# Performance work log

Hardware: AMD Instinct MI355X
Metric: run time of the kernel (lower is better)

The kernel has to match this reference:

```python
import jax, jax.numpy as jnp
import numpy as np

B, H = 8192, 768


def _mk_linear(key, fan_in, fan_out):
    k1, k2 = jax.random.split(key)
    lim = 1.0 / np.sqrt(fan_in)
    W = jax.random.uniform(k1, (fan_out, fan_in), jnp.float32, -lim, lim)
    b = jax.random.uniform(k2, (fan_out,), jnp.float32, -lim, lim)
    return W, b


def setup_inputs() -> dict:
    key = jax.random.key(0)
    ks = jax.random.split(key, 6)
    modal_a = jax.random.normal(ks[0], (B, H), jnp.float32)
    modal_b = jax.random.normal(ks[1], (B, H), jnp.float32)
    W1m, b1m = _mk_linear(ks[2], H, H)
    W2m, b2m = _mk_linear(ks[3], H, H)
    W1v, b1v = _mk_linear(ks[4], H, H)
    W2v, b2v = _mk_linear(ks[5], H, H)
    return {"modal_a": modal_a, "modal_b": modal_b,
            "W1m": W1m, "b1m": b1m, "W2m": W2m, "b2m": b2m,
            "W1v": W1v, "b1v": b1v, "W2v": W2v, "b2v": b2v}


def reference(modal_a, modal_b, W1m, b1m, W2m, b2m, W1v, b1v, W2v, b2v):
    # mlp_mu: Linear -> Tanh -> Linear
    mu = jnp.tanh(modal_a @ W1m.T + b1m) @ W2m.T + b2m              # [B,H]
    # mlp_logvar: Linear -> Tanh -> Linear -> Tanh
    logvar = jnp.tanh(jnp.tanh(modal_a @ W1v.T + b1v) @ W2v.T + b2v)  # [B,H]
    inv_var = jnp.exp(-logvar)

    positive = -(mu - modal_b) ** 2 * 0.5 * inv_var                  # [B,H]

    # mean_j (mu[j] - mu[i])^2 = E[mu^2] - 2*mu[i]*E[mu] + mu[i]^2  (per feature dim)
    # Algebraic reduction of the O(B^2*H) tile in the original code.
    mu_mean = jnp.mean(mu, axis=0)                                   # [H]
    mu_sq_mean = jnp.mean(mu * mu, axis=0)                           # [H]
    pair_sq = mu_sq_mean - 2.0 * mu * mu_mean + mu * mu              # [B,H]
    negative = -pair_sq * 0.5 * inv_var                              # [B,H]

    pos_sum = jnp.sum(positive, axis=-1)                             # [B]
    neg_sum = jnp.sum(negative, axis=-1)                             # [B]
    lld = jnp.mean(pos_sum)
    bound = jnp.mean(pos_sum - neg_sum)
    return (lld, bound)
```

## Files before the change

kernel.cpp:

```cpp
#include <hip/hip_runtime.h>
#include <hip/hip_fp8.h>
#include <math.h>

typedef float v4f __attribute__((ext_vector_type(4)));

static constexpr int Bn = 8192;
static constexpr int Hn = 768;
static constexpr float invB = 1.0f / 8192.0f;

__device__ __forceinline__ unsigned char cvt_e4m3(float x) {
    __hip_fp8_e4m3 t(x);
    return t.__x;
}

__device__ __forceinline__ unsigned pack4_e4m3(float4 f) {
    return (unsigned)cvt_e4m3(f.x)
         | ((unsigned)cvt_e4m3(f.y) << 8)
         | ((unsigned)cvt_e4m3(f.z) << 16)
         | ((unsigned)cvt_e4m3(f.w) << 24);
}

__device__ __forceinline__ float fast_tanh(float x) {
    float xc = fminf(fmaxf(x, -15.0f), 15.0f);
    float e = __expf(2.0f * xc);
    float r = __builtin_amdgcn_rcpf(e + 1.0f);
    return 1.0f - 2.0f * r;
}

__global__ void prep_w(const float* __restrict__ W1m, const float* __restrict__ W2m,
                       const float* __restrict__ W1v, const float* __restrict__ W2v,
                       unsigned char* __restrict__ W1m_f8, unsigned char* __restrict__ W2m_f8,
                       unsigned char* __restrict__ W1v_f8, unsigned char* __restrict__ W2v_f8,
                       float* __restrict__ zbuf, int nzero) {
    const int tid = blockIdx.x * blockDim.x + threadIdx.x;
    if (tid < nzero) zbuf[tid] = 0.0f;
    constexpr int W4 = Hn * Hn / 4;
    const int total = 4 * W4;
    const int stride = gridDim.x * blockDim.x;
    for (int i = tid; i < total; i += stride) {
        int w = i / W4, j = i - w * W4;
        const float* s = (w == 0) ? W1m : (w == 1) ? W2m : (w == 2) ? W1v : W2v;
        unsigned char* d = (w == 0) ? W1m_f8 : (w == 1) ? W2m_f8 : (w == 2) ? W1v_f8 : W2v_f8;
        float4 v = ((const float4*)s)[j];
        ((unsigned*)d)[j] = pack4_e4m3(v);
    }
}

__launch_bounds__(512, 2)
__global__ void club_fused(const float* __restrict__ A_g,
                           const unsigned char* __restrict__ W1m, const unsigned char* __restrict__ W1v,
                           const unsigned char* __restrict__ W2m, const unsigned char* __restrict__ W2v,
                           const float* __restrict__ b1m, const float* __restrict__ b1v,
                           const float* __restrict__ b2m, const float* __restrict__ b2v,
                           const float* __restrict__ mb,
                           float* __restrict__ cs, float* __restrict__ cs2,
                           float* __restrict__ siv, float* __restrict__ sivmu,
                           float* __restrict__ accum, float* __restrict__ outp) {
    __shared__ __align__(16) unsigned char Hm[32 * 768];
    __shared__ __align__(16) unsigned char Xs[32 * 768];
    const int t = threadIdx.x;
    const int strip0 = blockIdx.x * 32;

    {
        const int row = t >> 4, seg = t & 15;
        const float* src = A_g + (size_t)(strip0 + row) * Hn;
#pragma unroll
        for (int j = 0; j < 3; ++j) {
            const int c = seg + 16 * j;
            float4 f0 = *(const float4*)(src + c * 16 + 0);
            float4 f1 = *(const float4*)(src + c * 16 + 4);
            float4 f2 = *(const float4*)(src + c * 16 + 8);
            float4 f3 = *(const float4*)(src + c * 16 + 12);
            uint4 p;
            p.x = pack4_e4m3(f0); p.y = pack4_e4m3(f1);
            p.z = pack4_e4m3(f2); p.w = pack4_e4m3(f3);
            *(uint4*)&Xs[row * 768 + ((c ^ (row & 15)) << 4)] = p;
        }
    }
    __syncthreads();

    const int w = t >> 6, lane = t & 63;
    const int lr = lane & 15, quad = lane >> 4;
    const int wc0 = w * 96;

    v4f am[6][2] = {}, av[6][2] = {};
    {
        ulonglong2 Wm1[2][6], Wv1[2][6];
        const unsigned char* __restrict__ pWm = W1m + (size_t)(wc0 + lr) * Hn + quad * 16;
        const unsigned char* __restrict__ pWv = W1v + (size_t)(wc0 + lr) * Hn + quad * 16;

#define LDW1(s_, ms_) do {                                                                  \
    _Pragma("unroll")                                                                       \
    for (int ct = 0; ct < 6; ++ct) {                                                        \
        Wm1[s_][ct] = *(const ulonglong2*)(pWm + ct * (16 * Hn) + (ms_) * 64);              \
        Wv1[s_][ct] = *(const ulonglong2*)(pWv + ct * (16 * Hn) + (ms_) * 64);              \
    } } while (0)

#define FM1(s_, ms_) do {                                                                   \
    ulonglong2 Af[2];                                                                       \
    _Pragma("unroll")                                                                       \
    for (int rt = 0; rt < 2; ++rt) {                                                        \
        const int row_ = rt * 16 + lr;                                                      \
        const int k_ = (ms_) * 4 + quad;                                                    \
        Af[rt] = *(const ulonglong2*)&Xs[row_ * 768 + ((k_ ^ (row_ & 15)) << 4)];           \
    }                                                                                       \
    _Pragma("unroll")                                                                       \
    for (int ct = 0; ct < 6; ++ct)                                                          \
    _Pragma("unroll")                                                                       \
    for (int rt = 0; rt < 2; ++rt) {                                                        \
        am[ct][rt] = __builtin_amdgcn_mfma_f32_16x16x32_fp8_fp8((long)Wm1[s_][ct].x, (long)Af[rt].x, am[ct][rt], 0, 0, 0); \
        am[ct][rt] = __builtin_amdgcn_mfma_f32_16x16x32_fp8_fp8((long)Wm1[s_][ct].y, (long)Af[rt].y, am[ct][rt], 0, 0, 0); \
        av[ct][rt] = __builtin_amdgcn_mfma_f32_16x16x32_fp8_fp8((long)Wv1[s_][ct].x, (long)Af[rt].x, av[ct][rt], 0, 0, 0); \
        av[ct][rt] = __builtin_amdgcn_mfma_f32_16x16x32_fp8_fp8((long)Wv1[s_][ct].y, (long)Af[rt].y, av[ct][rt], 0, 0, 0); \
    } } while (0)

        LDW1(0, 0);
#pragma unroll
        for (int ms = 0; ms < 11; ++ms) {
            if ((ms & 1) == 0) { LDW1(1, ms + 1); FM1(0, ms); }
            else               { LDW1(0, ms + 1); FM1(1, ms); }
        }
        FM1(1, 11);
#undef LDW1
#undef FM1
    }

    __syncthreads();

#pragma unroll
    for (int ct = 0; ct < 6; ++ct) {
        const float4 bbm = *(const float4*)&b1m[wc0 + ct * 16 + quad * 4];
        const float4 bbv = *(const float4*)&b1v[wc0 + ct * 16 + quad * 4];
        const int cc = w * 6 + ct;
#pragma unroll
        for (int rt = 0; rt < 2; ++rt) {
            const int row = rt * 16 + lr;
            v4f a = am[ct][rt];
            unsigned pm = (unsigned)cvt_e4m3(fast_tanh(a[0] + bbm.x))
                        | ((unsigned)cvt_e4m3(fast_tanh(a[1] + bbm.y)) << 8)
                        | ((unsigned)cvt_e4m3(fast_tanh(a[2] + bbm.z)) << 16)
                        | ((unsigned)cvt_e4m3(fast_tanh(a[3] + bbm.w)) << 24);
            v4f b = av[ct][rt];
            unsigned pv = (unsigned)cvt_e4m3(fast_tanh(b[0] + bbv.x))
                        | ((unsigned)cvt_e4m3(fast_tanh(b[1] + bbv.y)) << 8)
                        | ((unsigned)cvt_e4m3(fast_tanh(b[2] + bbv.z)) << 16)
                        | ((unsigned)cvt_e4m3(fast_tanh(b[3] + bbv.w)) << 24);
            const int off = row * 768 + ((cc ^ (row & 15)) << 4) + quad * 4;
            *(unsigned*)&Hm[off] = pm;
            *(unsigned*)&Xs[off] = pv;
        }
    }
    __syncthreads();

    v4f cm[2][6] = {}, cv[2][6] = {};
    {
        ulonglong2 Wm2[2][6], Wv2[2][6];
        const unsigned char* __restrict__ pWm = W2m + (size_t)(wc0 + lr) * Hn + quad * 16;
        const unsigned char* __restrict__ pWv = W2v + (size_t)(wc0 + lr) * Hn + quad * 16;

#define LDW2(s_, ms_) do {                                                                  \
    _Pragma("unroll")                                                                       \
    for (int ct = 0; ct < 6; ++ct) {                                                        \
        Wm2[s_][ct] = *(const ulonglong2*)(pWm + ct * (16 * Hn) + (ms_) * 64);              \
        Wv2[s_][ct] = *(const ulonglong2*)(pWv + ct * (16 * Hn) + (ms_) * 64);              \
    } } while (0)

#define FM2(s_, ms_) do {                                                                   \
    ulonglong2 Am[2], Av[2];                                                                \
    _Pragma("unroll")                                                                       \
    for (int rt = 0; rt < 2; ++rt) {                                                        \
        const int row_ = rt * 16 + lr;                                                      \
        const int k_ = (ms_) * 4 + quad;                                                    \
        const int off_ = row_ * 768 + ((k_ ^ (row_ & 15)) << 4);                            \
        Am[rt] = *(const ulonglong2*)&Hm[off_];                                             \
        Av[rt] = *(const ulonglong2*)&Xs[off_];                                             \
    }                                                                                       \
    _Pragma("unroll")                                                                       \
    for (int rt = 0; rt < 2; ++rt)                                                          \
    _Pragma("unroll")                                                                       \
    for (int ct = 0; ct < 6; ++ct) {                                                        \
        cm[rt][ct] = __builtin_amdgcn_mfma_f32_16x16x32_fp8_fp8((long)Am[rt].x, (long)Wm2[s_][ct].x, cm[rt][ct], 0, 0, 0); \
        cm[rt][ct] = __builtin_amdgcn_mfma_f32_16x16x32_fp8_fp8((long)Am[rt].y, (long)Wm2[s_][ct].y, cm[rt][ct], 0, 0, 0); \
        cv[rt][ct] = __builtin_amdgcn_mfma_f32_16x16x32_fp8_fp8((long)Av[rt].x, (long)Wv2[s_][ct].x, cv[rt][ct], 0, 0, 0); \
        cv[rt][ct] = __builtin_amdgcn_mfma_f32_16x16x32_fp8_fp8((long)Av[rt].y, (long)Wv2[s_][ct].y, cv[rt][ct], 0, 0, 0); \
    } } while (0)

        LDW2(0, 0);
#pragma unroll
        for (int ms = 0; ms < 11; ++ms) {
            if ((ms & 1) == 0) { LDW2(1, ms + 1); FM2(0, ms); }
            else               { LDW2(0, ms + 1); FM2(1, ms); }
        }
        FM2(1, 11);
#undef LDW2
#undef FM2
    }

    float pos = 0.f, q = 0.f;
#pragma unroll
    for (int ct = 0; ct < 6; ++ct) {
        const int col = wc0 + ct * 16 + lr;
        const float bmc = b2m[col], bvc = b2v[col];
        float c1 = 0.f, c2 = 0.f, c3 = 0.f, c4 = 0.f;
#pragma unroll
        for (int rt = 0; rt < 2; ++rt) {
#pragma unroll
            for (int r = 0; r < 4; ++r) {
                const int row = strip0 + rt * 16 + quad * 4 + r;
                float mu = cm[rt][ct][r] + bmc;
                float tv = fast_tanh(cv[rt][ct][r] + bvc);
                float iv = __expf(-tv);
                float mbv = mb[(size_t)row * Hn + col];
                float d = mu - mbv;
                pos += iv * d * d;
                q   += iv * mu * mu;
                c1 += mu; c2 += mu * mu; c3 += iv; c4 += iv * mu;
            }
        }
        c1 += __shfl_xor(c1, 16); c1 += __shfl_xor(c1, 32);
        c2 += __shfl_xor(c2, 16); c2 += __shfl_xor(c2, 32);
        c3 += __shfl_xor(c3, 16); c3 += __shfl_xor(c3, 32);
        c4 += __shfl_xor(c4, 16); c4 += __shfl_xor(c4, 32);
        if (quad == 0) {
            atomicAdd(&cs[col], c1);
            atomicAdd(&cs2[col], c2);
            atomicAdd(&siv[col], c3);
            atomicAdd(&sivmu[col], c4);
        }
    }
    for (int off = 32; off > 0; off >>= 1) {
        pos += __shfl_down(pos, off);
        q   += __shfl_down(q, off);
    }
    __shared__ float redP[8], redQ[8];
    if (lane == 0) { redP[w] = pos; redQ[w] = q; }
    __syncthreads();
    __shared__ int is_last;
    if (t == 0) {
        float sp = 0.f, sq = 0.f;
#pragma unroll
        for (int i = 0; i < 8; ++i) { sp += redP[i]; sq += redQ[i]; }
        atomicAdd(&accum[0], sp);
        atomicAdd(&accum[1], sq);
        __threadfence();
        unsigned old = atomicAdd((unsigned int*)&accum[3], 1u);
        is_last = (old == gridDim.x - 1) ? 1 : 0;
    }
    __syncthreads();
    if (is_last) {
        float term = 0.f;
        for (int h = t; h < Hn; h += 512) {
            float v1 = atomicAdd(&cs[h], 0.0f);
            float v2 = atomicAdd(&cs2[h], 0.0f);
            float v3 = atomicAdd(&siv[h], 0.0f);
            float v4 = atomicAdd(&sivmu[h], 0.0f);
            term += v3 * v2 - 2.0f * v4 * v1;
        }
        for (int off = 32; off > 0; off >>= 1) term += __shfl_down(term, off);
        __shared__ float redT[8];
        if (lane == 0) redT[w] = term;
        __syncthreads();
        if (t == 0) {
            float T = 0.f;
#pragma unroll
            for (int i = 0; i < 8; ++i) T += redT[i];
            float P = atomicAdd(&accum[0], 0.0f);
            float Q = atomicAdd(&accum[1], 0.0f);
            float pos_sum = -0.5f * P;
            float neg_sum = -0.5f * (T * invB + Q);
            outp[0] = pos_sum * invB;
            outp[1] = (pos_sum - neg_sum) * invB;
        }
    }
}

extern "C" void kernel_launch(void* const* d_in, const int* in_sizes, int n_in,
                              void* d_out, int out_size, void* d_ws, size_t ws_size,
                              hipStream_t stream) {
    const float* modal_a = (const float*)d_in[0];
    const float* modal_b = (const float*)d_in[1];
    const float* W1m = (const float*)d_in[2];
    const float* b1m = (const float*)d_in[3];
    const float* W2m = (const float*)d_in[4];
    const float* b2m = (const float*)d_in[5];
    const float* W1v = (const float*)d_in[6];
    const float* b1v = (const float*)d_in[7];
    const float* W2v = (const float*)d_in[8];
    const float* b2v = (const float*)d_in[9];
    float* out = (float*)d_out;

    char* ws = (char*)d_ws;
    constexpr size_t szW8 = (size_t)Hn * Hn;
    unsigned char* W1m_f8 = (unsigned char*)(ws);
    unsigned char* W2m_f8 = (unsigned char*)(ws + szW8);
    unsigned char* W1v_f8 = (unsigned char*)(ws + 2 * szW8);
    unsigned char* W2v_f8 = (unsigned char*)(ws + 3 * szW8);
    float* cs     = (float*)(ws + 4 * szW8);
    float* cs2    = cs + Hn;
    float* siv    = cs + 2 * Hn;
    float* sivmu  = cs + 3 * Hn;
    float* accum  = cs + 4 * Hn;

    prep_w<<<576, 256, 0, stream>>>(W1m, W2m, W1v, W2v,
                                    W1m_f8, W2m_f8, W1v_f8, W2v_f8,
                                    cs, 4 * Hn + 8);

    club_fused<<<dim3(Bn / 32), 512, 0, stream>>>(
        modal_a, W1m_f8, W1v_f8, W2m_f8, W2v_f8,
        b1m, b1v, b2m, b2v, modal_b,
        cs, cs2, siv, sivmu, accum, out);
}
```

Before: 189.9 us.

## Double block to 1024 threads, halve per-wave column tiles, drop weight prefetch

Launches the fused kernel with 1024 threads (16 waves) per 32-row strip, so each wave owns 48 instead of 96 output columns. The explicit double-buffered weight register prefetch is removed in favor of simple per-step loads, cutting accumulator and prefetch register pressure to allow more waves per CU. Reductions and the strip load loop are adjusted for 16 waves. In exchange, global weight latency is less hidden within each wave and relies on more resident waves, and each wave reuses every A fragment across fewer column tiles.

```diff
diff --git a/kernel.cpp b/kernel.cpp
--- a/kernel.cpp
+++ b/kernel.cpp
@@ -46,7 +46,7 @@
     }
 }
 
-__launch_bounds__(512, 2)
+__launch_bounds__(1024, 4)
 __global__ void club_fused(const float* __restrict__ A_g,
                            const unsigned char* __restrict__ W1m, const unsigned char* __restrict__ W1v,
                            const unsigned char* __restrict__ W2m, const unsigned char* __restrict__ W2v,
@@ -61,77 +61,66 @@
     const int t = threadIdx.x;
     const int strip0 = blockIdx.x * 32;
 
-    {
-        const int row = t >> 4, seg = t & 15;
-        const float* src = A_g + (size_t)(strip0 + row) * Hn;
-#pragma unroll
-        for (int j = 0; j < 3; ++j) {
-            const int c = seg + 16 * j;
-            float4 f0 = *(const float4*)(src + c * 16 + 0);
-            float4 f1 = *(const float4*)(src + c * 16 + 4);
-            float4 f2 = *(const float4*)(src + c * 16 + 8);
-            float4 f3 = *(const float4*)(src + c * 16 + 12);
-            uint4 p;
-            p.x = pack4_e4m3(f0); p.y = pack4_e4m3(f1);
-            p.z = pack4_e4m3(f2); p.w = pack4_e4m3(f3);
-            *(uint4*)&Xs[row * 768 + ((c ^ (row & 15)) << 4)] = p;
-        }
+    for (int c = t; c < 1536; c += 1024) {
+        const int row = c / 48, cc = c - row * 48;
+        const float* src = A_g + (size_t)(strip0 + row) * Hn + cc * 16;
+        float4 f0 = *(const float4*)(src + 0);
+        float4 f1 = *(const float4*)(src + 4);
+        float4 f2 = *(const float4*)(src + 8);
+        float4 f3 = *(const float4*)(src + 12);
+        uint4 p;
+        p.x = pack4_e4m3(f0); p.y = pack4_e4m3(f1);
+        p.z = pack4_e4m3(f2); p.w = pack4_e4m3(f3);
+        *(uint4*)&Xs[row * 768 + ((cc ^ (row & 15)) << 4)] = p;
     }
     __syncthreads();
 
     const int w = t >> 6, lane = t & 63;
     const int lr = lane & 15, quad = lane >> 4;
-    const int wc0 = w * 96;
-
-    v4f am[6][2] = {}, av[6][2] = {};
+    const int wc0 = w * 48;
+
+    v4f am[3][2] = {}, av[3][2] = {};
     {
-        ulonglong2 Wm1[2][6], Wv1[2][6];
         const unsigned char* __restrict__ pWm = W1m + (size_t)(wc0 + lr) * Hn + quad * 16;
         const unsigned char* __restrict__ pWv = W1v + (size_t)(wc0 + lr) * Hn + quad * 16;
-
-#define LDW1(s_, ms_) do {                                                                  \
-    _Pragma("unroll")                                                                       \
-    for (int ct = 0; ct < 6; ++ct) {                                                        \
-        Wm1[s_][ct] = *(const ulonglong2*)(pWm + ct * (16 * Hn) + (ms_) * 64);              \
-        Wv1[s_][ct] = *(const ulonglong2*)(pWv + ct * (16 * Hn) + (ms_) * 64);              \
-    } } while (0)
-
-#define FM1(s_, ms_) do {                                                                   \
-    ulonglong2 Af[2];                                                                       \
-    _Pragma("unroll")                                                                       \
-    for (int rt = 0; rt < 2; ++rt) {                                                        \
-        const int row_ = rt * 16 + lr;                                                      \
-        const int k_ = (ms_) * 4 + quad;                                                    \
-        Af[rt] = *(const ulonglong2*)&Xs[row_ * 768 + ((k_ ^ (row_ & 15)) << 4)];           \
-    }                                                                                       \
-    _Pragma("unroll")                                                                       \
-    for (int ct = 0; ct < 6; ++ct)                                                          \
-    _Pragma("unroll")                                                                       \
-    for (int rt = 0; rt < 2; ++rt) {                                                        \
-        am[ct][rt] = __builtin_amdgcn_mfma_f32_16x16x32_fp8_fp8((long)Wm1[s_][ct].x, (long)Af[rt].x, am[ct][rt], 0, 0, 0); \
-        am[ct][rt] = __builtin_amdgcn_mfma_f32_16x16x32_fp8_fp8((long)Wm1[s_][ct].y, (long)Af[rt].y, am[ct][rt], 0, 0, 0); \
-        av[ct][rt] = __builtin_amdgcn_mfma_f32_16x16x32_fp8_fp8((long)Wv1[s_][ct].x, (long)Af[rt].x, av[ct][rt], 0, 0, 0); \
-        av[ct][rt] = __builtin_amdgcn_mfma_f32_16x16x32_fp8_fp8((long)Wv1[s_][ct].y, (long)Af[rt].y, av[ct][rt], 0, 0, 0); \
-    } } while (0)
-
-        LDW1(0, 0);
-#pragma unroll
-        for (int ms = 0; ms < 11; ++ms) {
-            if ((ms & 1) == 0) { LDW1(1, ms + 1); FM1(0, ms); }
-            else               { LDW1(0, ms + 1); FM1(1, ms); }
-        }
-        FM1(1, 11);
-#undef LDW1
-#undef FM1
-    }
-
-    __syncthreads();
-
-#pragma unroll
-    for (int ct = 0; ct < 6; ++ct) {
+#pragma unroll
+        for (int ms = 0; ms < 12; ++ms) {
+            ulonglong2 wmf[3], wvf[3], af[2];
+#pragma unroll
+            for (int ct = 0; ct < 3; ++ct) {
+                wmf[ct] = *(const ulonglong2*)(pWm + ct * (16 * Hn) + ms * 64);
+                wvf[ct] = *(const ulonglong2*)(pWv + ct * (16 * Hn) + ms * 64);
+            }
+#pragma unroll
+            for (int rt = 0; rt < 2; ++rt) {
+                const int row_ = rt * 16 + lr;
+                const int k_ = ms * 4 + quad;
+                af[rt] = *(const ulonglong2*)&Xs[row_ * 768 + ((k_ ^ (row_ & 15)) << 4)];
+            }
+#pragma unroll
+            for (int ct = 0; ct < 3; ++ct)
+#pragma unroll
+                for (int rt = 0; rt < 2; ++rt) {
+                    am[ct][rt] = __builtin_amdgcn_mfma_f32_16x16x32_fp8_fp8((long)wmf[ct].x, (long)af[rt].x, am[ct][rt], 0, 0, 0);
+                    av[ct][rt] = __builtin_amdgcn_mfma_f32_16x16x32_fp8_fp8((long)wvf[ct].x, (long)af[rt].x, av[ct][rt], 0, 0, 0);
+                }
+#pragma unroll
+            for (int ct = 0; ct < 3; ++ct)
+#pragma unroll
+                for (int rt = 0; rt < 2; ++rt) {
+                    am[ct][rt] = __builtin_amdgcn_mfma_f32_16x16x32_fp8_fp8((long)wmf[ct].y, (long)af[rt].y, am[ct][rt], 0, 0, 0);
+                    av[ct][rt] = __builtin_amdgcn_mfma_f32_16x16x32_fp8_fp8((long)wvf[ct].y, (long)af[rt].y, av[ct][rt], 0, 0, 0);
+                }
+        }
+    }
+
+    __syncthreads();
+
+#pragma unroll
+    for (int ct = 0; ct < 3; ++ct) {
         const float4 bbm = *(const float4*)&b1m[wc0 + ct * 16 + quad * 4];
         const float4 bbv = *(const float4*)&b1v[wc0 + ct * 16 + quad * 4];
-        const int cc = w * 6 + ct;
+        const int cc = w * 3 + ct;
 #pragma unroll
         for (int rt = 0; rt < 2; ++rt) {
             const int row = rt * 16 + lr;
@@ -152,53 +141,46 @@
     }
     __syncthreads();
 
-    v4f cm[2][6] = {}, cv[2][6] = {};
+    v4f cm[2][3] = {}, cv[2][3] = {};
     {
-        ulonglong2 Wm2[2][6], Wv2[2][6];
         const unsigned char* __restrict__ pWm = W2m + (size_t)(wc0 + lr) * Hn + quad * 16;
         const unsigned char* __restrict__ pWv = W2v + (size_t)(wc0 + lr) * Hn + quad * 16;
-
-#define LDW2(s_, ms_) do {                                                                  \
-    _Pragma("unroll")                                                                       \
-    for (int ct = 0; ct < 6; ++ct) {                                                        \
-        Wm2[s_][ct] = *(const ulonglong2*)(pWm + ct * (16 * Hn) + (ms_) * 64);              \
-        Wv2[s_][ct] = *(const ulonglong2*)(pWv + ct * (16 * Hn) + (ms_) * 64);              \
-    } } while (0)
-
-#define FM2(s_, ms_) do {                                                                   \
-    ulonglong2 Am[2], Av[2];                                                                \
-    _Pragma("unroll")                                                                       \
-    for (int rt = 0; rt < 2; ++rt) {                                                        \
-        const int row_ = rt * 16 + lr;                                                      \
-        const int k_ = (ms_) * 4 + quad;                                                    \
-        const int off_ = row_ * 768 + ((k_ ^ (row_ & 15)) << 4);                            \
-        Am[rt] = *(const ulonglong2*)&Hm[off_];                                             \
-        Av[rt] = *(const ulonglong2*)&Xs[off_];                                             \
-    }                                                                                       \
-    _Pragma("unroll")                                                                       \
-    for (int rt = 0; rt < 2; ++rt)                                                          \
-    _Pragma("unroll")                                                                       \
-    for (int ct = 0; ct < 6; ++ct) {                                                        \
-        cm[rt][ct] = __builtin_amdgcn_mfma_f32_16x16x32_fp8_fp8((long)Am[rt].x, (long)Wm2[s_][ct].x, cm[rt][ct], 0, 0, 0); \
-        cm[rt][ct] = __builtin_amdgcn_mfma_f32_16x16x32_fp8_fp8((long)Am[rt].y, (long)Wm2[s_][ct].y, cm[rt][ct], 0, 0, 0); \
-        cv[rt][ct] = __builtin_amdgcn_mfma_f32_16x16x32_fp8_fp8((long)Av[rt].x, (long)Wv2[s_][ct].x, cv[rt][ct], 0, 0, 0); \
-        cv[rt][ct] = __builtin_amdgcn_mfma_f32_16x16x32_fp8_fp8((long)Av[rt].y, (long)Wv2[s_][ct].y, cv[rt][ct], 0, 0, 0); \
-    } } while (0)
-
-        LDW2(0, 0);
-#pragma unroll
-        for (int ms = 0; ms < 11; ++ms) {
-            if ((ms & 1) == 0) { LDW2(1, ms + 1); FM2(0, ms); }
-            else               { LDW2(0, ms + 1); FM2(1, ms); }
-        }
-        FM2(1, 11);
-#undef LDW2
-#undef FM2
+#pragma unroll
+        for (int ms = 0; ms < 12; ++ms) {
+            ulonglong2 wmf[3], wvf[3], amf[2], avf[2];
+#pragma unroll
+            for (int ct = 0; ct < 3; ++ct) {
+                wmf[ct] = *(const ulonglong2*)(pWm + ct * (16 * Hn) + ms * 64);
+                wvf[ct] = *(const ulonglong2*)(pWv + ct * (16 * Hn) + ms * 64);
+            }
+#pragma unroll
+            for (int rt = 0; rt < 2; ++rt) {
+                const int row_ = rt * 16 + lr;
+                const int k_ = ms * 4 + quad;
+                const int off_ = row_ * 768 + ((k_ ^ (row_ & 15)) << 4);
+                amf[rt] = *(const ulonglong2*)&Hm[off_];
+                avf[rt] = *(const ulonglong2*)&Xs[off_];
+            }
+#pragma unroll
+            for (int rt = 0; rt < 2; ++rt)
+#pragma unroll
+                for (int ct = 0; ct < 3; ++ct) {
+                    cm[rt][ct] = __builtin_amdgcn_mfma_f32_16x16x32_fp8_fp8((long)amf[rt].x, (long)wmf[ct].x, cm[rt][ct], 0, 0, 0);
+                    cv[rt][ct] = __builtin_amdgcn_mfma_f32_16x16x32_fp8_fp8((long)avf[rt].x, (long)wvf[ct].x, cv[rt][ct], 0, 0, 0);
+                }
+#pragma unroll
+            for (int rt = 0; rt < 2; ++rt)
+#pragma unroll
+                for (int ct = 0; ct < 3; ++ct) {
+                    cm[rt][ct] = __builtin_amdgcn_mfma_f32_16x16x32_fp8_fp8((long)amf[rt].y, (long)wmf[ct].y, cm[rt][ct], 0, 0, 0);
+                    cv[rt][ct] = __builtin_amdgcn_mfma_f32_16x16x32_fp8_fp8((long)avf[rt].y, (long)wvf[ct].y, cv[rt][ct], 0, 0, 0);
+                }
+        }
     }
 
     float pos = 0.f, q = 0.f;
 #pragma unroll
-    for (int ct = 0; ct < 6; ++ct) {
+    for (int ct = 0; ct < 3; ++ct) {
         const int col = wc0 + ct * 16 + lr;
         const float bmc = b2m[col], bvc = b2v[col];
         float c1 = 0.f, c2 = 0.f, c3 = 0.f, c4 = 0.f;
@@ -232,14 +214,14 @@
         pos += __shfl_down(pos, off);
         q   += __shfl_down(q, off);
     }
-    __shared__ float redP[8], redQ[8];
+    __shared__ float redP[16], redQ[16];
     if (lane == 0) { redP[w] = pos; redQ[w] = q; }
     __syncthreads();
     __shared__ int is_last;
     if (t == 0) {
         float sp = 0.f, sq = 0.f;
 #pragma unroll
-        for (int i = 0; i < 8; ++i) { sp += redP[i]; sq += redQ[i]; }
+        for (int i = 0; i < 16; ++i) { sp += redP[i]; sq += redQ[i]; }
         atomicAdd(&accum[0], sp);
         atomicAdd(&accum[1], sq);
         __threadfence();
@@ -249,7 +231,7 @@
     __syncthreads();
     if (is_last) {
         float term = 0.f;
-        for (int h = t; h < Hn; h += 512) {
+        for (int h = t; h < Hn; h += 1024) {
             float v1 = atomicAdd(&cs[h], 0.0f);
             float v2 = atomicAdd(&cs2[h], 0.0f);
             float v3 = atomicAdd(&siv[h], 0.0f);
@@ -257,13 +239,13 @@
             term += v3 * v2 - 2.0f * v4 * v1;
         }
         for (int off = 32; off > 0; off >>= 1) term += __shfl_down(term, off);
-        __shared__ float redT[8];
+        __shared__ float redT[16];
         if (lane == 0) redT[w] = term;
         __syncthreads();
         if (t == 0) {
             float T = 0.f;
 #pragma unroll
-            for (int i = 0; i < 8; ++i) T += redT[i];
+            for (int i = 0; i < 16; ++i) T += redT[i];
             float P = atomicAdd(&accum[0], 0.0f);
             float Q = atomicAdd(&accum[1], 0.0f);
             float pos_sum = -0.5f * P;
@@ -305,7 +287,7 @@
                                     W1m_f8, W2m_f8, W1v_f8, W2v_f8,
                                     cs, 4 * Hn + 8);
 
-    club_fused<<<dim3(Bn / 32), 512, 0, stream>>>(
+    club_fused<<<dim3(Bn / 32), 1024, 0, stream>>>(
         modal_a, W1m_f8, W1v_f8, W2m_f8, W2v_f8,
         b1m, b1v, b2m, b2v, modal_b,
         cs, cs2, siv, sivmu, accum, out);
```

After: 188.0 us. About the same (-1.0%).
